# Optimization experiments

Measured on AMD Instinct MI355X. Metric: run time of the kernel, lower is better.

The kernel has to match this reference:

```python
import jax, jax.numpy as jnp
import numpy as np


def setup_inputs() -> dict:
    key = jax.random.key(0)
    k1, k2, k3 = jax.random.split(key, 3)
    B, N, M, S = 2, 8192, 32768, 4096
    pred = jax.random.normal(k1, (B, N, 3), dtype=jnp.float32)
    target = jax.random.normal(k2, (B, M, 3), dtype=jnp.float32)
    # stands in for torch.randperm(N)[:S]; duplicates don't change the math shape-wise
    idx = jax.random.randint(k3, (S,), 0, N, dtype=jnp.int64)
    return {"pred": pred, "target": target, "idx": idx}


def reference(pred, target, idx):
    # pred: (B, N, 3), target: (B, M, 3), idx: (S,)
    pred_s = pred[:, idx, :]                       # (B, S, 3) -- sampled points
    x2 = jnp.sum(pred_s * pred_s, axis=-1)         # (B, S)
    y2 = jnp.sum(target * target, axis=-1)         # (B, M)
    xy = jnp.einsum("bsd,bmd->bsm", pred_s, target)  # (B, S, M)
    d2 = x2[:, :, None] + y2[:, None, :] - 2.0 * xy
    dist = jnp.sqrt(jnp.maximum(d2, 0.0))          # (B, S, M)
    min_dist = jnp.min(dist, axis=2)               # (B, S)
    return jnp.mean(min_dist)
```

## Files before the change

kernel.cpp:

```cpp
#include <hip/hip_runtime.h>
#include <math.h>

typedef float vf2 __attribute__((ext_vector_type(2)));

constexpr int B = 2;
constexpr int N = 8192;
constexpr int M = 32768;
constexpr int S = 4096;
constexpr int QTOT = B * S;
constexpr int R = 16;
constexpr int WT = 64 * R;
constexpr int TCH = M / WT;
constexpr int QG = S / 64;
constexpr int WAVES = B * TCH * QG;
constexpr int BLOCKS = WAVES / 4;


__global__ __launch_bounds__(256) void chamfer_prep(
    const float* __restrict__ pred, const int* __restrict__ idx,
    float4* __restrict__ qrec, unsigned* __restrict__ wsmin) {
  int q = blockIdx.x * 256 + threadIdx.x;
  if (q >= QTOT) return;
  int b = q / S;
  int s = q - b * S;
  int i = idx[s];
  const float* p = pred + ((size_t)b * N + (size_t)i) * 3;
  float x = p[0], y = p[1], z = p[2];
  qrec[q] = make_float4(-2.0f * x, -2.0f * y, -2.0f * z,
                        x * x + y * y + z * z);
  wsmin[q] = 0x7F800000u;
}

__global__ __launch_bounds__(256) void chamfer_main(
    const float* __restrict__ target, const float4* __restrict__ qrec,
    unsigned* __restrict__ wsmin) {
  __shared__ float4 qs[64];
  const int lane = threadIdx.x & 63;
  const int w = blockIdx.x * 4 + (threadIdx.x >> 6);
  const int b = w >> 11;
  const int rem = w & 2047;
  const int tch = rem & (TCH - 1);
  const int qg = rem >> 5;

  if (threadIdx.x < 64)
    qs[threadIdx.x] = qrec[b * S + qg * 64 + threadIdx.x];

  const float* tb = target + ((size_t)b * M + (size_t)tch * WT) * 3;
  vf2 t0p[8], t1p[8], t2p[8], ty2p[8];
#pragma unroll
  for (int p = 0; p < 8; ++p) {
    int mA = (2 * p) * 64 + lane;
    int mB = (2 * p + 1) * 64 + lane;
    float ax = tb[3 * mA], ay = tb[3 * mA + 1], az = tb[3 * mA + 2];
    float bx = tb[3 * mB], by = tb[3 * mB + 1], bz = tb[3 * mB + 2];
    t0p[p] = vf2{ax, bx};
    t1p[p] = vf2{ay, by};
    t2p[p] = vf2{az, bz};
    ty2p[p] = vf2{fmaf(ax, ax, fmaf(ay, ay, az * az)),
                  fmaf(bx, bx, fmaf(by, by, bz * bz))};
  }
  __syncthreads();

  const float qx2_home = qs[lane].w;
  const int rot = ((lane + 1) & 63) * 4;
  float mm = INFINITY;
  int qoff = lane;

  for (int step = 0; step < 64; ++step) {
    float4 qr = qs[qoff];
    vf2 q0 = vf2{qr.x, qr.x}, q1 = vf2{qr.y, qr.y}, q2 = vf2{qr.z, qr.z};
    float m0 = mm, m1 = INFINITY;
#pragma unroll
    for (int p = 0; p < 8; p += 2) {
      vf2 s = __builtin_elementwise_fma(q0, t0p[p], ty2p[p]);
      s = __builtin_elementwise_fma(q1, t1p[p], s);
      s = __builtin_elementwise_fma(q2, t2p[p], s);
      m0 = fminf(fminf(s.x, s.y), m0);
      vf2 u = __builtin_elementwise_fma(q0, t0p[p + 1], ty2p[p + 1]);
      u = __builtin_elementwise_fma(q1, t1p[p + 1], u);
      u = __builtin_elementwise_fma(q2, t2p[p + 1], u);
      m1 = fminf(fminf(u.x, u.y), m1);
    }
    mm = fminf(m0, m1);
    mm = __int_as_float(__builtin_amdgcn_ds_bpermute(rot, __float_as_int(mm)));
    qoff = (qoff + 1) & 63;
  }
  const int q = b * S + qg * 64 + lane;
  atomicMin(&wsmin[q], __float_as_uint(fmaxf(qx2_home + mm, 0.0f)));
}

__global__ __launch_bounds__(1024) void chamfer_finish(
    const unsigned* __restrict__ wsmin, float* __restrict__ out) {
  __shared__ float red[16];
  float sum = 0.0f;
  for (int q = threadIdx.x; q < QTOT; q += 1024)
    sum += sqrtf(__uint_as_float(wsmin[q]));
#pragma unroll
  for (int off = 32; off > 0; off >>= 1)
    sum += __shfl_down(sum, off, 64);
  int wv = threadIdx.x >> 6;
  if ((threadIdx.x & 63) == 0) red[wv] = sum;
  __syncthreads();
  if (threadIdx.x == 0) {
    float t = 0.0f;
#pragma unroll
    for (int i = 0; i < 16; ++i) t += red[i];
    out[0] = t / (float)QTOT;
  }
}

extern "C" void kernel_launch(void* const* d_in, const int* in_sizes, int n_in,
                              void* d_out, int out_size, void* d_ws, size_t ws_size,
                              hipStream_t stream) {
  const float* pred = (const float*)d_in[0];
  const float* target = (const float*)d_in[1];
  const int* idx = (const int*)d_in[2];
  unsigned* wsmin = (unsigned*)d_ws;
  float4* qrec = (float4*)((char*)d_ws + 32 * 1024);

  chamfer_prep<<<QTOT / 256, 256, 0, stream>>>(pred, idx, qrec, wsmin);
  chamfer_main<<<BLOCKS, 256, 0, stream>>>(target, qrec, wsmin);
  chamfer_finish<<<1, 1024, 0, stream>>>(wsmin, (float*)d_out);
}
```

Measured before the change: 84.50 us.

## Double per-lane target register tile and fold query prep into main kernel

Result: no change. 83.47 us (-1.2%).

```diff
diff --git a/kernel.cpp b/kernel.cpp
--- a/kernel.cpp
+++ b/kernel.cpp
@@ -8,7 +8,7 @@
 constexpr int M = 32768;
 constexpr int S = 4096;
 constexpr int QTOT = B * S;
-constexpr int R = 16;
+constexpr int R = 32;
 constexpr int WT = 64 * R;
 constexpr int TCH = M / WT;
 constexpr int QG = S / 64;
@@ -16,39 +16,32 @@
 constexpr int BLOCKS = WAVES / 4;
 
 
-__global__ __launch_bounds__(256) void chamfer_prep(
-    const float* __restrict__ pred, const int* __restrict__ idx,
-    float4* __restrict__ qrec, unsigned* __restrict__ wsmin) {
-  int q = blockIdx.x * 256 + threadIdx.x;
-  if (q >= QTOT) return;
-  int b = q / S;
-  int s = q - b * S;
-  int i = idx[s];
-  const float* p = pred + ((size_t)b * N + (size_t)i) * 3;
-  float x = p[0], y = p[1], z = p[2];
-  qrec[q] = make_float4(-2.0f * x, -2.0f * y, -2.0f * z,
-                        x * x + y * y + z * z);
-  wsmin[q] = 0x7F800000u;
-}
-
-__global__ __launch_bounds__(256) void chamfer_main(
-    const float* __restrict__ target, const float4* __restrict__ qrec,
-    unsigned* __restrict__ wsmin) {
-  __shared__ float4 qs[64];
+__global__ __launch_bounds__(256, 2) void chamfer_main(
+    const float* __restrict__ pred, const float* __restrict__ target,
+    const int* __restrict__ idx, unsigned* __restrict__ wsmin) {
+  __shared__ float qs0[64], qs1[64], qs2[64], qw[64];
   const int lane = threadIdx.x & 63;
   const int w = blockIdx.x * 4 + (threadIdx.x >> 6);
-  const int b = w >> 11;
-  const int rem = w & 2047;
+  const int b = w >> 10;
+  const int rem = w & 1023;
   const int tch = rem & (TCH - 1);
-  const int qg = rem >> 5;
+  const int qg = rem >> 4;
 
-  if (threadIdx.x < 64)
-    qs[threadIdx.x] = qrec[b * S + qg * 64 + threadIdx.x];
+  if (threadIdx.x < 64) {
+    int s = qg * 64 + threadIdx.x;
+    int i = idx[s];
+    const float* p = pred + ((size_t)b * N + (size_t)i) * 3;
+    float x = p[0], y = p[1], z = p[2];
+    qs0[threadIdx.x] = -2.0f * x;
+    qs1[threadIdx.x] = -2.0f * y;
+    qs2[threadIdx.x] = -2.0f * z;
+    qw[threadIdx.x] = x * x + y * y + z * z;
+  }
 
   const float* tb = target + ((size_t)b * M + (size_t)tch * WT) * 3;
-  vf2 t0p[8], t1p[8], t2p[8], ty2p[8];
+  vf2 t0p[16], t1p[16], t2p[16], ty2p[16];
 #pragma unroll
-  for (int p = 0; p < 8; ++p) {
+  for (int p = 0; p < 16; ++p) {
     int mA = (2 * p) * 64 + lane;
     int mB = (2 * p + 1) * 64 + lane;
     float ax = tb[3 * mA], ay = tb[3 * mA + 1], az = tb[3 * mA + 2];
@@ -61,17 +54,18 @@
   }
   __syncthreads();
 
-  const float qx2_home = qs[lane].w;
+  const float qx2_home = qw[lane];
   const int rot = ((lane + 1) & 63) * 4;
   float mm = INFINITY;
   int qoff = lane;
 
   for (int step = 0; step < 64; ++step) {
-    float4 qr = qs[qoff];
-    vf2 q0 = vf2{qr.x, qr.x}, q1 = vf2{qr.y, qr.y}, q2 = vf2{qr.z, qr.z};
+    vf2 q0 = vf2{qs0[qoff], qs0[qoff]};
+    vf2 q1 = vf2{qs1[qoff], qs1[qoff]};
+    vf2 q2 = vf2{qs2[qoff], qs2[qoff]};
     float m0 = mm, m1 = INFINITY;
 #pragma unroll
-    for (int p = 0; p < 8; p += 2) {
+    for (int p = 0; p < 16; p += 2) {
       vf2 s = __builtin_elementwise_fma(q0, t0p[p], ty2p[p]);
       s = __builtin_elementwise_fma(q1, t1p[p], s);
       s = __builtin_elementwise_fma(q2, t2p[p], s);
@@ -116,9 +110,8 @@
   const float* target = (const float*)d_in[1];
   const int* idx = (const int*)d_in[2];
   unsigned* wsmin = (unsigned*)d_ws;
-  float4* qrec = (float4*)((char*)d_ws + 32 * 1024);
 
-  chamfer_prep<<<QTOT / 256, 256, 0, stream>>>(pred, idx, qrec, wsmin);
-  chamfer_main<<<BLOCKS, 256, 0, stream>>>(target, qrec, wsmin);
+  hipMemsetAsync(wsmin, 0x7F, QTOT * sizeof(unsigned), stream);
+  chamfer_main<<<BLOCKS, 256, 0, stream>>>(pred, target, idx, wsmin);
   chamfer_finish<<<1, 1024, 0, stream>>>(wsmin, (float*)d_out);
 }
```
